# Kernel tuning notes

Measured on AMD Instinct MI355X. Metric: run time of the kernel, lower is better.

Reference implementation:

```python
import jax, jax.numpy as jnp
import numpy as np

LN_EPS = 1e-5

def setup_inputs() -> dict:
    key = jax.random.key(0)
    ks = jax.random.split(key, 10)
    B, L, D2 = 64, 512, 16  # batch, max_len_text, 2*n_degree
    V, D, C = 8000, 256, 4  # n_word, d_model, n_category
    E = (V - 1) * V + 1      # edge-weight table size
    x = jax.random.randint(ks[0], (B, L), 0, V, dtype=jnp.int32)
    nb_x = jax.random.randint(ks[1], (B, L, D2), 0, V, dtype=jnp.int32)
    w_edge = jax.random.randint(ks[2], (B, L, D2), 0, E, dtype=jnp.int32)
    emb_weight = jax.random.normal(ks[3], (V, D), jnp.float32) * 0.02
    emb_weight = emb_weight.at[0].set(0.0)  # padding_idx=0
    w_edge_table = jax.random.normal(ks[4], (E, 1), jnp.float32) * 0.02
    w_edge_table = w_edge_table.at[0].set(0.0)
    eta_table = jax.random.normal(ks[5], (V, 1), jnp.float32) * 0.02
    eta_table = eta_table.at[0].set(0.0)
    ln_gamma = jnp.ones((D,), jnp.float32)
    ln_beta = jnp.zeros((D,), jnp.float32)
    fc_w = jax.random.normal(ks[6], (D, C), jnp.float32) * 0.02
    fc_b = jnp.zeros((C,), jnp.float32)
    return {"x": x, "nb_x": nb_x, "w_edge": w_edge,
            "emb_weight": emb_weight, "w_edge_table": w_edge_table,
            "eta_table": eta_table, "ln_gamma": ln_gamma, "ln_beta": ln_beta,
            "fc_w": fc_w, "fc_b": fc_b}

def _layernorm(h, gamma, beta):
    mu = jnp.mean(h, axis=-1, keepdims=True)
    var = jnp.mean(jnp.square(h - mu), axis=-1, keepdims=True)
    return (h - mu) * jax.lax.rsqrt(var + LN_EPS) * gamma + beta

def reference(x, nb_x, w_edge, emb_weight, w_edge_table, eta_table,
              ln_gamma, ln_beta, fc_w, fc_b):
    # idx_nodes: (B, L, 2*deg + 1) -- neighbors then self
    idx_nodes = jnp.concatenate([nb_x, x[..., None]], axis=-1)
    emb_nodes = emb_weight[idx_nodes]                  # (B, L, 2d+1, D)
    emb_nodes = _layernorm(emb_nodes, ln_gamma, ln_beta)
    we = w_edge_table[w_edge]                          # (B, L, 2d, 1)
    msg_nb = jnp.max(we * emb_nodes[:, :, :-1, :], axis=2)  # (B, L, D)
    eta = eta_table[x]                                 # (B, L, 1)
    h_node = (1.0 - eta) * msg_nb + eta * emb_nodes[:, :, -1, :]
    scores = h_node.sum(axis=1) @ fc_w + fc_b          # (B, C)
    return scores
```

## Files before the change

### kernel.cpp

```cpp
#include <hip/hip_runtime.h>
#include <math.h>

#define DV   256
#define BB   64
#define LL   512
#define DEG2 16
#define VV   8000
#define CC   4
#define LPW  4
#define NQ   (LL/LPW)
#define NE   (BB*LL*DEG2)
#define LN_EPS 1e-5f

typedef _Float16 half4 __attribute__((ext_vector_type(4)));
typedef float    f32x4 __attribute__((ext_vector_type(4)));

__global__ void __launch_bounds__(64) ln_rows_kernel(
    const float* __restrict__ emb, const float* __restrict__ gamma,
    const float* __restrict__ beta,
    const int* __restrict__ w_edge, const float* __restrict__ we_table,
    half4* __restrict__ out, float* __restrict__ we_flat)
{
    const int row = blockIdx.x;
    const int ln  = threadIdx.x;

    for (int g = blockIdx.x * 64 + ln; g < NE; g += VV * 64)
        we_flat[g] = we_table[w_edge[g]];

    const f32x4 v = ((const f32x4*)(emb + row * DV))[ln];

    float s = v[0] + v[1] + v[2] + v[3];
    #pragma unroll
    for (int off = 32; off > 0; off >>= 1) s += __shfl_xor(s, off);
    const float mu = s * (1.0f / DV);

    f32x4 c;
    #pragma unroll
    for (int k = 0; k < 4; ++k) c[k] = v[k] - mu;

    float q = c[0]*c[0] + c[1]*c[1] + c[2]*c[2] + c[3]*c[3];
    #pragma unroll
    for (int off = 32; off > 0; off >>= 1) q += __shfl_xor(q, off);
    const float rs = rsqrtf(q * (1.0f / DV) + LN_EPS);

    const f32x4 g  = ((const f32x4*)gamma)[ln];
    const f32x4 bt = ((const f32x4*)beta)[ln];

    half4 h;
    #pragma unroll
    for (int k = 0; k < 4; ++k) h[k] = (_Float16)(c[k] * rs * g[k] + bt[k]);
    out[row * 64 + ln] = h;
}

__global__ void __launch_bounds__(128) gnn_wave_kernel(
    const int*   __restrict__ nb_x,
    const int*   __restrict__ x,
    const float* __restrict__ we_flat,
    const float* __restrict__ eta_table,
    const half4* __restrict__ norm_emb,
    float*       __restrict__ h_part)
{
    const int tid = threadIdx.x;
    const int ln  = tid & 63;
    const int wid = blockIdx.x * 2 + (tid >> 6);
    const int b   = wid >> 7;
    const int lq  = wid & 127;

    const int l0   = lq * LPW;
    const int base = b * LL + l0;

    const int   nbv = __builtin_nontemporal_load(nb_x    + base * DEG2 + ln);
    const float wev = __builtin_nontemporal_load(we_flat + base * DEG2 + ln);

    int xv = 0; float etv = 0.0f;
    if (ln < LPW) { xv = x[base + ln]; etv = eta_table[xv]; }

    f32x4 acc = {0.0f, 0.0f, 0.0f, 0.0f};

    #pragma unroll
    for (int li = 0; li < LPW; ++li) {
        half4 m;
        m[0] = m[1] = m[2] = m[3] = (_Float16)(-65504.0f);

        #pragma unroll
        for (int j = 0; j < DEG2; ++j) {
            const int   lane = li * DEG2 + j;
            const int   idx  = __shfl(nbv, lane);
            const float wej  = __shfl(wev, lane);
            half4 w4; w4[0] = w4[1] = w4[2] = w4[3] = (_Float16)wej;
            const half4 e = norm_emb[idx * 64 + ln];
            m = __builtin_elementwise_max(m, w4 * e);
        }

        const int   sidx = __shfl(xv, li);
        const float eta  = __shfl(etv, li);
        const half4 se   = norm_emb[sidx * 64 + ln];
        const float om   = 1.0f - eta;
        #pragma unroll
        for (int k = 0; k < 4; ++k)
            acc[k] += om * (float)m[k] + eta * (float)se[k];
    }

    __builtin_nontemporal_store(acc,
        (f32x4*)(h_part + (size_t)(b * NQ + lq) * DV) + ln);
}

__global__ void __launch_bounds__(256) fc_kernel(
    const float* __restrict__ h_part,
    const float* __restrict__ fc_w,
    const float* __restrict__ fc_b,
    float*       __restrict__ out)
{
    const int b  = blockIdx.x;
    const int d  = threadIdx.x;
    const int w  = d >> 6;
    const int ln = d & 63;

    float h = 0.0f;
    #pragma unroll 8
    for (int lq = 0; lq < NQ; ++lq)
        h += h_part[(size_t)(b * NQ + lq) * DV + d];

    float p[CC];
    #pragma unroll
    for (int c = 0; c < CC; ++c) p[c] = h * fc_w[d * CC + c];

    #pragma unroll
    for (int c = 0; c < CC; ++c)
        #pragma unroll
        for (int off = 32; off > 0; off >>= 1) p[c] += __shfl_xor(p[c], off);

    __shared__ float s_red[4][CC];
    if (ln == 0) {
        #pragma unroll
        for (int c = 0; c < CC; ++c) s_red[w][c] = p[c];
    }
    __syncthreads();
    if (d < CC)
        out[b * CC + d] = s_red[0][d] + s_red[1][d] + s_red[2][d] + s_red[3][d] + fc_b[d];
}

extern "C" void kernel_launch(void* const* d_in, const int* in_sizes, int n_in,
                              void* d_out, int out_size, void* d_ws, size_t ws_size,
                              hipStream_t stream) {
    const int*   x        = (const int*)  d_in[0];
    const int*   nb_x     = (const int*)  d_in[1];
    const int*   w_edge   = (const int*)  d_in[2];
    const float* emb_w    = (const float*)d_in[3];
    const float* we_table = (const float*)d_in[4];
    const float* eta_tab  = (const float*)d_in[5];
    const float* ln_gamma = (const float*)d_in[6];
    const float* ln_beta  = (const float*)d_in[7];
    const float* fc_w     = (const float*)d_in[8];
    const float* fc_b     = (const float*)d_in[9];
    float* out = (float*)d_out;

    char* ws = (char*)d_ws;
    half4* norm_emb = (half4*)(ws);
    float* we_flat  = (float*)(ws + 4096000);
    float* h_part   = (float*)(ws + 4096000 + 2097152);

    ln_rows_kernel<<<VV, 64, 0, stream>>>(emb_w, ln_gamma, ln_beta,
                                          w_edge, we_table, norm_emb, we_flat);

    gnn_wave_kernel<<<BB * NQ / 2, 128, 0, stream>>>(
        nb_x, x, we_flat, eta_tab, norm_emb, h_part);

    fc_kernel<<<BB, 256, 0, stream>>>(h_part, fc_w, fc_b, out);
}
```

Measured before the change: 49.54 us.

## Fuse FC projection into GNN kernel with block reduction and atomic adds

Removes the separate FC kernel and the h_part workspace round trip. Each 256-thread block now covers 16 positions of one batch row and reduces its four wave accumulators in shared memory. It applies the FC weights and atomically adds its per-category partials into the output, which the LN kernel pre-initializes with the bias. This saves one launch and the partial-sum write and read. In exchange it adds atomics, a block sync, and a dependency on the LN kernel initializing the output.

Result: faster. 42.26 us (-14.7%).

```diff
diff --git a/kernel.cpp b/kernel.cpp
--- a/kernel.cpp
+++ b/kernel.cpp
@@ -8,7 +8,8 @@
 #define VV   8000
 #define CC   4
 #define LPW  4
-#define NQ   (LL/LPW)
+#define NW   4
+#define NLC  32
 #define NE   (BB*LL*DEG2)
 #define LN_EPS 1e-5f
 
@@ -19,10 +20,17 @@
     const float* __restrict__ emb, const float* __restrict__ gamma,
     const float* __restrict__ beta,
     const int* __restrict__ w_edge, const float* __restrict__ we_table,
-    half4* __restrict__ out, float* __restrict__ we_flat)
+    const float* __restrict__ fc_b,
+    half4* __restrict__ out_tab, float* __restrict__ we_flat,
+    float* __restrict__ out)
 {
     const int row = blockIdx.x;
     const int ln  = threadIdx.x;
+
+    if (row == 0) {
+        #pragma unroll
+        for (int i = ln; i < BB * CC; i += 64) out[i] = fc_b[i & 3];
+    }
 
     for (int g = blockIdx.x * 64 + ln; g < NE; g += VV * 64)
         we_flat[g] = we_table[w_edge[g]];
@@ -49,24 +57,25 @@
     half4 h;
     #pragma unroll
     for (int k = 0; k < 4; ++k) h[k] = (_Float16)(c[k] * rs * g[k] + bt[k]);
-    out[row * 64 + ln] = h;
+    out_tab[row * 64 + ln] = h;
 }
 
-__global__ void __launch_bounds__(128) gnn_wave_kernel(
+__global__ void __launch_bounds__(256) gnn_kernel(
     const int*   __restrict__ nb_x,
     const int*   __restrict__ x,
     const float* __restrict__ we_flat,
     const float* __restrict__ eta_table,
     const half4* __restrict__ norm_emb,
-    float*       __restrict__ h_part)
+    const float* __restrict__ fc_w,
+    float*       __restrict__ out)
 {
+    const int b   = blockIdx.x;
+    const int lc  = blockIdx.y;
     const int tid = threadIdx.x;
+    const int w   = tid >> 6;
     const int ln  = tid & 63;
-    const int wid = blockIdx.x * 2 + (tid >> 6);
-    const int b   = wid >> 7;
-    const int lq  = wid & 127;
 
-    const int l0   = lq * LPW;
+    const int l0   = lc * 16 + w * LPW;
     const int base = b * LL + l0;
 
     const int   nbv = __builtin_nontemporal_load(nb_x    + base * DEG2 + ln);
@@ -101,43 +110,39 @@
             acc[k] += om * (float)m[k] + eta * (float)se[k];
     }
 
-    __builtin_nontemporal_store(acc,
-        (f32x4*)(h_part + (size_t)(b * NQ + lq) * DV) + ln);
-}
+    __shared__ float s_acc[NW][DV];
+    ((f32x4*)s_acc[w])[ln] = acc;
+    __syncthreads();
+    if (w == 0) {
+        f32x4 r0 = ((f32x4*)s_acc[0])[ln];
+        f32x4 r1 = ((f32x4*)s_acc[1])[ln];
+        f32x4 r2 = ((f32x4*)s_acc[2])[ln];
+        f32x4 r3 = ((f32x4*)s_acc[3])[ln];
+        f32x4 h;
+        #pragma unroll
+        for (int k = 0; k < 4; ++k) h[k] = r0[k] + r1[k] + r2[k] + r3[k];
 
-__global__ void __launch_bounds__(256) fc_kernel(
-    const float* __restrict__ h_part,
-    const float* __restrict__ fc_w,
-    const float* __restrict__ fc_b,
-    float*       __restrict__ out)
-{
-    const int b  = blockIdx.x;
-    const int d  = threadIdx.x;
-    const int w  = d >> 6;
-    const int ln = d & 63;
+        const f32x4 w0 = ((const f32x4*)fc_w)[ln * 4 + 0];
+        const f32x4 w1 = ((const f32x4*)fc_w)[ln * 4 + 1];
+        const f32x4 w2 = ((const f32x4*)fc_w)[ln * 4 + 2];
+        const f32x4 w3 = ((const f32x4*)fc_w)[ln * 4 + 3];
 
-    float h = 0.0f;
-    #pragma unroll 8
-    for (int lq = 0; lq < NQ; ++lq)
-        h += h_part[(size_t)(b * NQ + lq) * DV + d];
+        float p[CC];
+        #pragma unroll
+        for (int c = 0; c < CC; ++c)
+            p[c] = h[0] * w0[c] + h[1] * w1[c] + h[2] * w2[c] + h[3] * w3[c];
 
-    float p[CC];
-    #pragma unroll
-    for (int c = 0; c < CC; ++c) p[c] = h * fc_w[d * CC + c];
+        #pragma unroll
+        for (int c = 0; c < CC; ++c)
+            #pragma unroll
+            for (int off = 32; off > 0; off >>= 1) p[c] += __shfl_xor(p[c], off);
 
-    #pragma unroll
-    for (int c = 0; c < CC; ++c)
-        #pragma unroll
-        for (int off = 32; off > 0; off >>= 1) p[c] += __shfl_xor(p[c], off);
-
-    __shared__ float s_red[4][CC];
-    if (ln == 0) {
-        #pragma unroll
-        for (int c = 0; c < CC; ++c) s_red[w][c] = p[c];
+        if (ln == 0) {
+            #pragma unroll
+            for (int c = 0; c < CC; ++c)
+                atomicAdd(&out[b * CC + c], p[c]);
+        }
     }
-    __syncthreads();
-    if (d < CC)
-        out[b * CC + d] = s_red[0][d] + s_red[1][d] + s_red[2][d] + s_red[3][d] + fc_b[d];
 }
 
 extern "C" void kernel_launch(void* const* d_in, const int* in_sizes, int n_in,
@@ -158,13 +163,12 @@
     char* ws = (char*)d_ws;
     half4* norm_emb = (half4*)(ws);
     float* we_flat  = (float*)(ws + 4096000);
-    float* h_part   = (float*)(ws + 4096000 + 2097152);
 
     ln_rows_kernel<<<VV, 64, 0, stream>>>(emb_w, ln_gamma, ln_beta,
-                                          w_edge, we_table, norm_emb, we_flat);
+                                          w_edge, we_table, fc_b,
+                                          norm_emb, we_flat, out);
 
-    gnn_wave_kernel<<<BB * NQ / 2, 128, 0, stream>>>(
-        nb_x, x, we_flat, eta_tab, norm_emb, h_part);
-
-    fc_kernel<<<BB, 256, 0, stream>>>(h_part, fc_w, fc_b, out);
+    dim3 grid2(BB, NLC);
+    gnn_kernel<<<grid2, 256, 0, stream>>>(nb_x, x, we_flat, eta_tab,
+                                          norm_emb, fc_w, out);
 }
```
